# Kernel tuning notes

Hardware: AMD Instinct MI355X
Metric: run time of the kernel (lower is better)

Reference implementation:

```python
import jax, jax.numpy as jnp
import numpy as np

B, N, D = 32, 2048, 2048
NORM_EPS = 1e-12   # torch F.normalize eps
COS_EPS = 1e-8     # torch cosine_similarity eps


def _l2_normalize(x):
    n = jnp.linalg.norm(x, axis=-1, keepdims=True)
    return x / jnp.maximum(n, NORM_EPS)


def setup_inputs() -> dict:
    key = jax.random.key(0)
    ks = jax.random.split(key, 5)
    q1 = jax.random.normal(ks[0], (B, D), dtype=jnp.float32)
    k1 = jax.random.normal(ks[1], (B, N, D), dtype=jnp.float32)
    q2 = jax.random.normal(ks[2], (B, D), dtype=jnp.float32)
    k2 = jax.random.normal(ks[3], (B, N, D), dtype=jnp.float32)
    mask = jax.random.uniform(ks[4], (B, N), dtype=jnp.float32)
    temp = 0.4 * jnp.ones((1,), dtype=jnp.float32)  # learned scalar param (unused in fwd math)
    return {"q1": q1, "k1": k1, "q2": q2, "k2": k2, "mask": mask, "temp": temp}


def reference(q1, k1, q2, k2, mask, temp):
    # L2-normalize along feature dim (torch F.normalize)
    q1n = _l2_normalize(q1)            # [B, D]
    k1n = _l2_normalize(k1)            # [B, N, D]
    # cosine similarity of q1n[:, None, :] vs k1n along last dim
    dot = jnp.einsum('bd,bnd->bn', q1n, k1n)  # [B, N]
    denom = jnp.maximum(
        jnp.linalg.norm(q1n, axis=-1)[:, None] * jnp.linalg.norm(k1n, axis=-1),
        COS_EPS,
    )
    scores = dot / denom               # [B, N] (norms ~1, faithful to torch)
    scores = scores * mask
    scores = jnp.clip(scores, 0.0, 1.0)
    return jax.nn.softmax(scores, axis=-1)
```

## Files before the change

kernel.cpp:

```cpp
#include <hip/hip_runtime.h>
#include <math.h>

#define BB 32
#define NN 2048
#define DD 2048

__global__ __launch_bounds__(256) void score_kernel(
    const float* __restrict__ q1,
    const float* __restrict__ k1,
    const float* __restrict__ mask,
    float* __restrict__ scores)
{
    __shared__ float q_lds[DD];

    const int block  = blockIdx.x;
    const int b      = block >> 9;
    const int n_base = (block & 511) << 2;
    const int tid    = threadIdx.x;

    const float4* q4  = (const float4*)(q1 + (size_t)b * DD);
    float4*       ql4 = (float4*)q_lds;
    ql4[tid]       = q4[tid];
    ql4[tid + 256] = q4[tid + 256];
    __syncthreads();

    const int wave = tid >> 6;
    const int lane = tid & 63;
    const int n    = n_base + wave;

    const float4* krow = (const float4*)(k1 + ((size_t)b * NN + n) * (size_t)DD);

    float dot = 0.0f, ksq = 0.0f, qsq = 0.0f;
#pragma unroll
    for (int it = 0; it < 8; ++it) {
        float4 kv = krow[it * 64 + lane];
        float4 qv = ql4 [it * 64 + lane];
        dot = fmaf(qv.x, kv.x, dot);
        dot = fmaf(qv.y, kv.y, dot);
        dot = fmaf(qv.z, kv.z, dot);
        dot = fmaf(qv.w, kv.w, dot);
        ksq = fmaf(kv.x, kv.x, ksq);
        ksq = fmaf(kv.y, kv.y, ksq);
        ksq = fmaf(kv.z, kv.z, ksq);
        ksq = fmaf(kv.w, kv.w, ksq);
        qsq = fmaf(qv.x, qv.x, qsq);
        qsq = fmaf(qv.y, qv.y, qsq);
        qsq = fmaf(qv.z, qv.z, qsq);
        qsq = fmaf(qv.w, qv.w, qsq);
    }

#pragma unroll
    for (int off = 1; off < 64; off <<= 1) {
        dot += __shfl_xor(dot, off);
        ksq += __shfl_xor(ksq, off);
        qsq += __shfl_xor(qsq, off);
    }

    if (lane == 0) {
        float nq = sqrtf(qsq);
        float nk = sqrtf(ksq);
        float s  = dot / (fmaxf(nq, 1e-12f) * fmaxf(nk, 1e-12f));
        s *= mask[b * NN + n];
        s  = fminf(fmaxf(s, 0.0f), 1.0f);
        scores[b * NN + n] = s;
    }
}

__global__ __launch_bounds__(256) void softmax_kernel(float* __restrict__ inout)
{
    const int b   = blockIdx.x;
    const int tid = threadIdx.x;
    const int wave = tid >> 6;
    const int lane = tid & 63;
    float* row = inout + (size_t)b * NN;

    __shared__ float red_max[4];
    __shared__ float red_sum[4];

    float v[8];
    float m = -INFINITY;
#pragma unroll
    for (int i = 0; i < 8; ++i) {
        v[i] = row[tid + i * 256];
        m = fmaxf(m, v[i]);
    }
#pragma unroll
    for (int off = 1; off < 64; off <<= 1)
        m = fmaxf(m, __shfl_xor(m, off));
    if (lane == 0) red_max[wave] = m;
    __syncthreads();
    m = fmaxf(fmaxf(red_max[0], red_max[1]), fmaxf(red_max[2], red_max[3]));

    float s = 0.0f;
#pragma unroll
    for (int i = 0; i < 8; ++i) {
        v[i] = expf(v[i] - m);
        s += v[i];
    }
#pragma unroll
    for (int off = 1; off < 64; off <<= 1)
        s += __shfl_xor(s, off);
    if (lane == 0) red_sum[wave] = s;
    __syncthreads();
    s = (red_sum[0] + red_sum[1]) + (red_sum[2] + red_sum[3]);

    float inv = 1.0f / s;
#pragma unroll
    for (int i = 0; i < 8; ++i)
        row[tid + i * 256] = v[i] * inv;
}

extern "C" void kernel_launch(void* const* d_in, const int* in_sizes, int n_in,
                              void* d_out, int out_size, void* d_ws, size_t ws_size,
                              hipStream_t stream) {
    const float* q1   = (const float*)d_in[0];
    const float* k1   = (const float*)d_in[1];
    const float* mask = (const float*)d_in[4];
    float* out = (float*)d_out;

    dim3 grid_score(BB * (NN / 4));
    score_kernel<<<grid_score, 256, 0, stream>>>(q1, k1, mask, out);
    softmax_kernel<<<BB, 256, 0, stream>>>(out);
}
```

Measured before the change: 93.78 us.

## Fuse exp and partial sums into score kernel, add nontemporal k loads

```diff
diff --git a/kernel.cpp b/kernel.cpp
--- a/kernel.cpp
+++ b/kernel.cpp
@@ -5,36 +5,39 @@
 #define NN 2048
 #define DD 2048
 
+typedef float f4v __attribute__((ext_vector_type(4)));
+
 __global__ __launch_bounds__(256) void score_kernel(
     const float* __restrict__ q1,
     const float* __restrict__ k1,
     const float* __restrict__ mask,
-    float* __restrict__ scores)
+    float* __restrict__ out,
+    float* __restrict__ partial)
 {
-    __shared__ float q_lds[DD];
+    __shared__ f4v  q_lds[DD / 4];
+    __shared__ float sm[4];
 
     const int block  = blockIdx.x;
     const int b      = block >> 9;
     const int n_base = (block & 511) << 2;
     const int tid    = threadIdx.x;
 
-    const float4* q4  = (const float4*)(q1 + (size_t)b * DD);
-    float4*       ql4 = (float4*)q_lds;
-    ql4[tid]       = q4[tid];
-    ql4[tid + 256] = q4[tid + 256];
+    const f4v* q4 = (const f4v*)(q1 + (size_t)b * DD);
+    q_lds[tid]       = q4[tid];
+    q_lds[tid + 256] = q4[tid + 256];
     __syncthreads();
 
     const int wave = tid >> 6;
     const int lane = tid & 63;
     const int n    = n_base + wave;
 
-    const float4* krow = (const float4*)(k1 + ((size_t)b * NN + n) * (size_t)DD);
+    const f4v* krow = (const f4v*)(k1 + ((size_t)b * NN + n) * (size_t)DD);
 
     float dot = 0.0f, ksq = 0.0f, qsq = 0.0f;
 #pragma unroll
     for (int it = 0; it < 8; ++it) {
-        float4 kv = krow[it * 64 + lane];
-        float4 qv = ql4 [it * 64 + lane];
+        f4v kv = __builtin_nontemporal_load(krow + it * 64 + lane);
+        f4v qv = q_lds[it * 64 + lane];
         dot = fmaf(qv.x, kv.x, dot);
         dot = fmaf(qv.y, kv.y, dot);
         dot = fmaf(qv.z, kv.z, dot);
@@ -62,52 +65,40 @@
         float s  = dot / (fmaxf(nq, 1e-12f) * fmaxf(nk, 1e-12f));
         s *= mask[b * NN + n];
         s  = fminf(fmaxf(s, 0.0f), 1.0f);
-        scores[b * NN + n] = s;
+        float e = expf(s);
+        out[b * NN + n] = e;
+        sm[wave] = e;
     }
+    __syncthreads();
+    if (tid == 0)
+        partial[block] = (sm[0] + sm[1]) + (sm[2] + sm[3]);
 }
 
-__global__ __launch_bounds__(256) void softmax_kernel(float* __restrict__ inout)
+__global__ __launch_bounds__(256) void scale_kernel(
+    float* __restrict__ out,
+    const float* __restrict__ partial)
 {
-    const int b   = blockIdx.x;
-    const int tid = threadIdx.x;
+    const int blk  = blockIdx.x;
+    const int b    = blk >> 3;
+    const int seg  = blk & 7;
+    const int tid  = threadIdx.x;
     const int wave = tid >> 6;
     const int lane = tid & 63;
-    float* row = inout + (size_t)b * NN;
 
-    __shared__ float red_max[4];
-    __shared__ float red_sum[4];
+    __shared__ float red[4];
 
-    float v[8];
-    float m = -INFINITY;
-#pragma unroll
-    for (int i = 0; i < 8; ++i) {
-        v[i] = row[tid + i * 256];
-        m = fmaxf(m, v[i]);
-    }
-#pragma unroll
-    for (int off = 1; off < 64; off <<= 1)
-        m = fmaxf(m, __shfl_xor(m, off));
-    if (lane == 0) red_max[wave] = m;
-    __syncthreads();
-    m = fmaxf(fmaxf(red_max[0], red_max[1]), fmaxf(red_max[2], red_max[3]));
-
-    float s = 0.0f;
-#pragma unroll
-    for (int i = 0; i < 8; ++i) {
-        v[i] = expf(v[i] - m);
-        s += v[i];
-    }
+    const float* p = partial + b * 512;
+    float s = p[tid] + p[tid + 256];
 #pragma unroll
     for (int off = 1; off < 64; off <<= 1)
         s += __shfl_xor(s, off);
-    if (lane == 0) red_sum[wave] = s;
+    if (lane == 0) red[wave] = s;
     __syncthreads();
-    s = (red_sum[0] + red_sum[1]) + (red_sum[2] + red_sum[3]);
+    float total = (red[0] + red[1]) + (red[2] + red[3]);
 
-    float inv = 1.0f / s;
-#pragma unroll
-    for (int i = 0; i < 8; ++i)
-        row[tid + i * 256] = v[i] * inv;
+    float inv = 1.0f / total;
+    const int n = seg * 256 + tid;
+    out[(size_t)b * NN + n] *= inv;
 }
 
 extern "C" void kernel_launch(void* const* d_in, const int* in_sizes, int n_in,
@@ -116,9 +107,10 @@
     const float* q1   = (const float*)d_in[0];
     const float* k1   = (const float*)d_in[1];
     const float* mask = (const float*)d_in[4];
-    float* out = (float*)d_out;
+    float* out     = (float*)d_out;
+    float* partial = (float*)d_ws;
 
     dim3 grid_score(BB * (NN / 4));
-    score_kernel<<<grid_score, 256, 0, stream>>>(q1, k1, mask, out);
-    softmax_kernel<<<BB, 256, 0, stream>>>(out);
+    score_kernel<<<grid_score, 256, 0, stream>>>(q1, k1, mask, out, partial);
+    scale_kernel<<<BB * 8, 256, 0, stream>>>(out, partial);
 }
```

Measured after the change: 83.82 us. -10.6%, faster.
